# Performance work log

Hardware: AMD Instinct MI355X
Metric: run time of the kernel (lower is better)

## Reference

```python
import jax, jax.numpy as jnp
import numpy as np

P, OBS, H, MSG, EMB, A = 2048, 512, 2048, 16, 32, 3
SLOPE = 0.01  # LeakyReLU default negative slope


def setup_inputs() -> dict:
    key = jax.random.key(0)
    ks = jax.random.split(key, 12)
    s = 0.02
    return {
        "obs": jax.random.normal(ks[0], (P, OBS), jnp.float32),
        "messages": jnp.zeros((P, MSG), jnp.float32),
        "embeddings": jnp.zeros((P, EMB), jnp.float32),
        "h": jnp.zeros((1, H), jnp.float32),
        "w_ih": jax.random.normal(ks[1], (3 * H, OBS), jnp.float32) * s,
        "w_hh": jax.random.normal(ks[2], (3 * H, H), jnp.float32) * s,
        "b_ih": jax.random.normal(ks[3], (3 * H,), jnp.float32) * s,
        "b_hh": jax.random.normal(ks[4], (3 * H,), jnp.float32) * s,
        "ff_w": jax.random.normal(ks[5], (2, H), jnp.float32) * s,
        "ff_b": jnp.zeros((2,), jnp.float32),
        "ap_w": jax.random.normal(ks[6], (A, H), jnp.float32) * s,
        "ap_b": jnp.zeros((A,), jnp.float32),
        "dp_w": jax.random.normal(ks[7], (A, H), jnp.float32) * s,
        "dp_b": jnp.zeros((A,), jnp.float32),
        "v_w": jax.random.normal(ks[8], (1, H), jnp.float32) * s,
        "v_b": jnp.zeros((1,), jnp.float32),
    }


def reference(obs, messages, embeddings, h, w_ih, w_hh, b_ih, b_hh,
              ff_w, ff_b, ap_w, ap_b, dp_w, dp_b, v_w, v_b):
    # h arg is ignored (module re-initializes it to zeros).
    hid = w_hh.shape[1]
    # precompute input-side GRU gates for all players: [P, 3H]
    gi_all = obs @ w_ih.T + b_ih

    def step(hc, gi):  # hc: [H]
        gh = hc @ w_hh.T + b_hh
        ir, iz, inn = jnp.split(gi, 3)
        hr, hz, hn = jnp.split(gh, 3)
        r = jax.nn.sigmoid(ir + hr)
        z = jax.nn.sigmoid(iz + hz)
        n = jnp.tanh(inn + r * hn)
        h_new = (1.0 - z) * n + z * hc
        return h_new, h_new

    h0 = jnp.zeros((hid,), obs.dtype)
    _, hs = jax.lax.scan(step, h0, gi_all)  # [P, H]

    acts = hs @ ff_w.T + ff_b                      # [P, 2]
    acts = jnp.where(acts >= 0, acts, SLOPE * acts)  # LeakyReLU
    a_w = jax.nn.softmax(acts[:, 0])               # softmax over players
    d_w = jax.nn.softmax(acts[:, 1])
    a_att = a_w @ hs                               # [H]
    d_att = d_w @ hs
    a_pol = a_att @ ap_w.T + ap_b
    d_pol = d_att @ dp_w.T + dp_b
    v = (a_att + d_att) @ v_w.T + v_b
    return (a_pol, d_pol, v)
```

## Files before the change

kernel.cpp:

```cpp
#include <hip/hip_runtime.h>
#include <cstdint>
#include <cstddef>

#define P_N  2048
#define OBS_N 512
#define H_N  2048
#define G3H  6144

__device__ __forceinline__ float wave_sum(float v) {
#pragma unroll
  for (int off = 32; off > 0; off >>= 1) v += __shfl_xor(v, off);
  return v;
}
__device__ __forceinline__ float wave_max(float v) {
#pragma unroll
  for (int off = 32; off > 0; off >>= 1) v = fmaxf(v, __shfl_xor(v, off));
  return v;
}

__global__ __launch_bounds__(256, 2) void gi_gemm(
    const float* __restrict__ A,
    const float* __restrict__ B,
    const float* __restrict__ bias,
    float* __restrict__ C)
{
  constexpr int BM = 128, BK = 32, LDP = BM + 4;
  __shared__ float As[BK][LDP];
  __shared__ float Bs[BK][LDP];
  const int tid = threadIdx.x;
  const int bm = blockIdx.y * BM;
  const int bn = blockIdx.x * BM;
  const int tx = tid & 15, ty = tid >> 4;
  const int lrow = tid >> 3;
  const int lk4  = (tid & 7) << 2;

  float acc[8][8];
#pragma unroll
  for (int i = 0; i < 8; ++i)
#pragma unroll
    for (int j = 0; j < 8; ++j) acc[i][j] = 0.f;

  for (int k0 = 0; k0 < OBS_N; k0 += BK) {
#pragma unroll
    for (int i = 0; i < 4; ++i) {
      const int r = lrow + 32 * i;
      float4 av = *(const float4*)(A + (size_t)(bm + r) * OBS_N + k0 + lk4);
      float4 bv = *(const float4*)(B + (size_t)(bn + r) * OBS_N + k0 + lk4);
      As[lk4 + 0][r] = av.x; As[lk4 + 1][r] = av.y;
      As[lk4 + 2][r] = av.z; As[lk4 + 3][r] = av.w;
      Bs[lk4 + 0][r] = bv.x; Bs[lk4 + 1][r] = bv.y;
      Bs[lk4 + 2][r] = bv.z; Bs[lk4 + 3][r] = bv.w;
    }
    __syncthreads();
#pragma unroll
    for (int k = 0; k < BK; ++k) {
      float4 a0 = *(const float4*)&As[k][ty * 4];
      float4 a1 = *(const float4*)&As[k][64 + ty * 4];
      float4 b0 = *(const float4*)&Bs[k][tx * 4];
      float4 b1 = *(const float4*)&Bs[k][64 + tx * 4];
      float a[8] = {a0.x, a0.y, a0.z, a0.w, a1.x, a1.y, a1.z, a1.w};
      float b[8] = {b0.x, b0.y, b0.z, b0.w, b1.x, b1.y, b1.z, b1.w};
#pragma unroll
      for (int i = 0; i < 8; ++i)
#pragma unroll
        for (int j = 0; j < 8; ++j)
          acc[i][j] = fmaf(a[i], b[j], acc[i][j]);
    }
    __syncthreads();
  }

  float4 bs0 = *(const float4*)(bias + bn + tx * 4);
  float4 bs1 = *(const float4*)(bias + bn + 64 + tx * 4);
  const float bb[8] = {bs0.x, bs0.y, bs0.z, bs0.w, bs1.x, bs1.y, bs1.z, bs1.w};
#pragma unroll
  for (int i = 0; i < 8; ++i) {
    const int row = bm + ((i < 4) ? (ty * 4 + i) : (64 + ty * 4 + i - 4));
    float4 o0 = {acc[i][0] + bb[0], acc[i][1] + bb[1], acc[i][2] + bb[2], acc[i][3] + bb[3]};
    float4 o1 = {acc[i][4] + bb[4], acc[i][5] + bb[5], acc[i][6] + bb[6], acc[i][7] + bb[7]};
    *(float4*)(C + (size_t)row * G3H + bn + tx * 4) = o0;
    *(float4*)(C + (size_t)row * G3H + bn + 64 + tx * 4) = o1;
  }
}

#define AGW(reg, val) \
  asm volatile("v_accvgpr_write_b32 " reg ", %0" :: "v"(val) : reg)
#define AGR(reg, dst) \
  asm volatile("v_accvgpr_read_b32 %0, " reg : "=v"(dst) :: reg)

#define LOADK_(koff, r0a,r0b,r0c,r0d, r1a,r1b,r1c,r1d, r2a,r2b,r2c,r2d) do { \
    float4 A_ = *(const float4*)(p0 + (koff) * 256 + l4); \
    float4 B_ = *(const float4*)(p1 + (koff) * 256 + l4); \
    float4 C_ = *(const float4*)(p2 + (koff) * 256 + l4); \
    AGW(r0a, A_.x); AGW(r0b, A_.y); AGW(r0c, A_.z); AGW(r0d, A_.w); \
    AGW(r1a, B_.x); AGW(r1b, B_.y); AGW(r1c, B_.z); AGW(r1d, B_.w); \
    AGW(r2a, C_.x); AGW(r2b, C_.y); AGW(r2c, C_.z); AGW(r2d, C_.w); \
  } while (0)

#define GEMVK_(koff, r0a,r0b,r0c,r0d, r1a,r1b,r1c,r1d, r2a,r2b,r2c,r2d) do { \
    float4 hv = *(const float4*)&hbuf[(koff) * 256 + l4]; \
    float tw; \
    AGR(r0a, tw); acc0 = fmaf(tw, hv.x, acc0); \
    AGR(r0b, tw); acc0 = fmaf(tw, hv.y, acc0); \
    AGR(r0c, tw); acc0 = fmaf(tw, hv.z, acc0); \
    AGR(r0d, tw); acc0 = fmaf(tw, hv.w, acc0); \
    AGR(r1a, tw); acc1 = fmaf(tw, hv.x, acc1); \
    AGR(r1b, tw); acc1 = fmaf(tw, hv.y, acc1); \
    AGR(r1c, tw); acc1 = fmaf(tw, hv.z, acc1); \
    AGR(r1d, tw); acc1 = fmaf(tw, hv.w, acc1); \
    AGR(r2a, tw); acc2 = fmaf(tw, hv.x, acc2); \
    AGR(r2b, tw); acc2 = fmaf(tw, hv.y, acc2); \
    AGR(r2c, tw); acc2 = fmaf(tw, hv.z, acc2); \
    AGR(r2d, tw); acc2 = fmaf(tw, hv.w, acc2); \
  } while (0)

#define LOADK(...) LOADK_(__VA_ARGS__)
#define GEMVK(...) GEMVK_(__VA_ARGS__)

#define KL0 "a0","a1","a2","a3",    "a32","a33","a34","a35", "a64","a65","a66","a67"
#define KL1 "a4","a5","a6","a7",    "a36","a37","a38","a39", "a68","a69","a70","a71"
#define KL2 "a8","a9","a10","a11",  "a40","a41","a42","a43", "a72","a73","a74","a75"
#define KL3 "a12","a13","a14","a15","a44","a45","a46","a47", "a76","a77","a78","a79"
#define KL4 "a16","a17","a18","a19","a48","a49","a50","a51", "a80","a81","a82","a83"
#define KL5 "a20","a21","a22","a23","a52","a53","a54","a55", "a84","a85","a86","a87"
#define KL6 "a24","a25","a26","a27","a56","a57","a58","a59", "a88","a89","a90","a91"
#define KL7 "a28","a29","a30","a31","a60","a61","a62","a63", "a92","a93","a94","a95"

__global__ __launch_bounds__(512, 1) void gru_scan(
    const float* __restrict__ w_hh,
    const float* __restrict__ b_hh,
    const float* __restrict__ gi,
    float* __restrict__ hs,
    unsigned long long* mb)
{
  __shared__ __align__(16) float hbuf[H_N];
  const int g   = blockIdx.x;
  const int tid = threadIdx.x;
  const int w   = tid >> 6;
  const int l   = tid & 63;
  const int l4  = l * 4;
  const int j   = (g << 3) + w;
  const int seg = (w << 8) + l;

  {
    const float* p0 = w_hh + (size_t)j * H_N;
    const float* p1 = w_hh + (size_t)(H_N + j) * H_N;
    const float* p2 = w_hh + (size_t)(2 * H_N + j) * H_N;
    LOADK(0, KL0); LOADK(1, KL1); LOADK(2, KL2); LOADK(3, KL3);
    LOADK(4, KL4); LOADK(5, KL5); LOADK(6, KL6); LOADK(7, KL7);
  }
  const float bh0 = b_hh[j], bh1 = b_hh[H_N + j], bh2 = b_hh[2 * H_N + j];
  float hprev = 0.f;

  for (int t = 0; t < P_N; ++t) {
    const float ir  = gi[(size_t)t * G3H + j];
    const float iz  = gi[(size_t)t * G3H + H_N + j];
    const float inn = gi[(size_t)t * G3H + 2 * H_N + j];

    float acc0 = 0.f, acc1 = 0.f, acc2 = 0.f;
    if (t > 0) {
      const unsigned tag = (unsigned)t;
      unsigned long long* base = mb + (size_t)((t - 1) & 1) * H_N + seg;
      float v0, v1, v2, v3;
      for (;;) {
        unsigned long long a0 =
            __hip_atomic_load(base +   0, __ATOMIC_RELAXED, __HIP_MEMORY_SCOPE_AGENT);
        unsigned long long a1 =
            __hip_atomic_load(base +  64, __ATOMIC_RELAXED, __HIP_MEMORY_SCOPE_AGENT);
        unsigned long long a2 =
            __hip_atomic_load(base + 128, __ATOMIC_RELAXED, __HIP_MEMORY_SCOPE_AGENT);
        unsigned long long a3 =
            __hip_atomic_load(base + 192, __ATOMIC_RELAXED, __HIP_MEMORY_SCOPE_AGENT);
        bool ok = ((unsigned)(a0 >> 32) == tag) & ((unsigned)(a1 >> 32) == tag) &
                  ((unsigned)(a2 >> 32) == tag) & ((unsigned)(a3 >> 32) == tag);
        if (__all(ok)) {
          v0 = __uint_as_float((unsigned)a0);
          v1 = __uint_as_float((unsigned)a1);
          v2 = __uint_as_float((unsigned)a2);
          v3 = __uint_as_float((unsigned)a3);
          break;
        }
        __builtin_amdgcn_s_sleep(1);
      }
      __syncthreads();
      hbuf[seg +   0] = v0;
      hbuf[seg +  64] = v1;
      hbuf[seg + 128] = v2;
      hbuf[seg + 192] = v3;
      __syncthreads();

      if (g == ((t - 1) & 255)) {
        *(float4*)(hs + (size_t)(t - 1) * H_N + tid * 4) =
            *(const float4*)&hbuf[tid * 4];
      }

      GEMVK(0, KL0); GEMVK(1, KL1); GEMVK(2, KL2); GEMVK(3, KL3);
      GEMVK(4, KL4); GEMVK(5, KL5); GEMVK(6, KL6); GEMVK(7, KL7);

#pragma unroll
      for (int off = 32; off > 0; off >>= 1) {
        acc0 += __shfl_xor(acc0, off);
        acc1 += __shfl_xor(acc1, off);
        acc2 += __shfl_xor(acc2, off);
      }
    }

    const float r = 1.f / (1.f + __expf(-(ir + acc0 + bh0)));
    const float z = 1.f / (1.f + __expf(-(iz + acc1 + bh1)));
    const float narg = inn + r * (acc2 + bh2);
    const float e2 = __expf(2.f * narg);
    const float n = (e2 - 1.f) / (e2 + 1.f);
    const float hnew = (1.f - z) * n + z * hprev;
    hprev = hnew;

    if (l == 0) {
      unsigned long long pk = ((unsigned long long)(unsigned)(t + 1) << 32) |
                              (unsigned long long)__float_as_uint(hnew);
      __hip_atomic_store(mb + (size_t)(t & 1) * H_N + j, pk,
                         __ATOMIC_RELAXED, __HIP_MEMORY_SCOPE_AGENT);
    }
  }

  if (l == 0) hs[(size_t)(P_N - 1) * H_N + j] = hprev;
}

__global__ __launch_bounds__(512) void acts_kernel(
    const float* __restrict__ hs, const float* __restrict__ ff_w,
    const float* __restrict__ ff_b, float* __restrict__ acts)
{
  const int w = threadIdx.x >> 6, l = threadIdx.x & 63;
  const int p = blockIdx.x * 8 + w;
  const float* hrow = hs + (size_t)p * H_N;
  float sa = 0.f, sd = 0.f;
#pragma unroll
  for (int k = 0; k < 8; ++k) {
    float4 hv = *(const float4*)(hrow + k * 256 + l * 4);
    float4 fa = *(const float4*)(ff_w + k * 256 + l * 4);
    float4 fd = *(const float4*)(ff_w + H_N + k * 256 + l * 4);
    sa += hv.x * fa.x + hv.y * fa.y + hv.z * fa.z + hv.w * fa.w;
    sd += hv.x * fd.x + hv.y * fd.y + hv.z * fd.z + hv.w * fd.w;
  }
  sa = wave_sum(sa); sd = wave_sum(sd);
  if (l == 0) {
    float a = sa + ff_b[0];
    float d = sd + ff_b[1];
    a = (a >= 0.f) ? a : 0.01f * a;
    d = (d >= 0.f) ? d : 0.01f * d;
    acts[p] = a;
    acts[P_N + p] = d;
  }
}

__global__ __launch_bounds__(256) void softmax_kernel(
    const float* __restrict__ acts, float* __restrict__ wts)
{
  __shared__ float red[4];
  __shared__ float bcast;
  const int tid = threadIdx.x;
  const int w = tid >> 6, l = tid & 63;
  for (int c = 0; c < 2; ++c) {
    const float* x = acts + c * P_N;
    float* y = wts + c * P_N;
    float m = -3.4e38f;
    for (int i = tid; i < P_N; i += 256) m = fmaxf(m, x[i]);
    m = wave_max(m);
    if (l == 0) red[w] = m;
    __syncthreads();
    if (tid == 0) bcast = fmaxf(fmaxf(red[0], red[1]), fmaxf(red[2], red[3]));
    __syncthreads();
    const float M = bcast;
    float s = 0.f;
    for (int i = tid; i < P_N; i += 256) {
      float e = __expf(x[i] - M);
      y[i] = e;
      s += e;
    }
    s = wave_sum(s);
    __syncthreads();
    if (l == 0) red[w] = s;
    __syncthreads();
    if (tid == 0) bcast = 1.f / (red[0] + red[1] + red[2] + red[3]);
    __syncthreads();
    const float inv = bcast;
    for (int i = tid; i < P_N; i += 256) y[i] *= inv;
    __syncthreads();
  }
}

__global__ __launch_bounds__(256) void pool_kernel(
    const float* __restrict__ hs, const float* __restrict__ wts,
    float* __restrict__ att)
{
  const int g = blockIdx.x;
  const int tid = threadIdx.x;
  const int c0 = tid * 8;
  float aa[8] = {0, 0, 0, 0, 0, 0, 0, 0};
  float dd[8] = {0, 0, 0, 0, 0, 0, 0, 0};
  for (int r = 0; r < 16; ++r) {
    const int p = g * 16 + r;
    const float wa = wts[p];
    const float wd = wts[P_N + p];
    const float* hp = hs + (size_t)p * H_N + c0;
    float4 h0 = *(const float4*)hp;
    float4 h1 = *(const float4*)(hp + 4);
    aa[0] = fmaf(wa, h0.x, aa[0]); aa[1] = fmaf(wa, h0.y, aa[1]);
    aa[2] = fmaf(wa, h0.z, aa[2]); aa[3] = fmaf(wa, h0.w, aa[3]);
    aa[4] = fmaf(wa, h1.x, aa[4]); aa[5] = fmaf(wa, h1.y, aa[5]);
    aa[6] = fmaf(wa, h1.z, aa[6]); aa[7] = fmaf(wa, h1.w, aa[7]);
    dd[0] = fmaf(wd, h0.x, dd[0]); dd[1] = fmaf(wd, h0.y, dd[1]);
    dd[2] = fmaf(wd, h0.z, dd[2]); dd[3] = fmaf(wd, h0.w, dd[3]);
    dd[4] = fmaf(wd, h1.x, dd[4]); dd[5] = fmaf(wd, h1.y, dd[5]);
    dd[6] = fmaf(wd, h1.z, dd[6]); dd[7] = fmaf(wd, h1.w, dd[7]);
  }
#pragma unroll
  for (int q = 0; q < 8; ++q) {
    atomicAdd(&att[c0 + q], aa[q]);
    atomicAdd(&att[H_N + c0 + q], dd[q]);
  }
}

__global__ __launch_bounds__(512) void head_kernel(
    const float* __restrict__ att,
    const float* __restrict__ ap_w, const float* __restrict__ ap_b,
    const float* __restrict__ dp_w, const float* __restrict__ dp_b,
    const float* __restrict__ v_w, const float* __restrict__ v_b,
    float* __restrict__ out)
{
  const int w = threadIdx.x >> 6, l = threadIdx.x & 63;
  if (w >= 7) return;
  float s = 0.f;
  if (w < 3) {
    const float* m = ap_w + (size_t)w * H_N;
    for (int k = 0; k < 32; ++k) { int i = k * 64 + l; s += att[i] * m[i]; }
  } else if (w < 6) {
    const float* m = dp_w + (size_t)(w - 3) * H_N;
    for (int k = 0; k < 32; ++k) { int i = k * 64 + l; s += att[H_N + i] * m[i]; }
  } else {
    for (int k = 0; k < 32; ++k) { int i = k * 64 + l; s += (att[i] + att[H_N + i]) * v_w[i]; }
  }
  s = wave_sum(s);
  if (l == 0) {
    float b = (w < 3) ? ap_b[w] : ((w < 6) ? dp_b[w - 3] : v_b[0]);
    out[w] = s + b;
  }
}

extern "C" void kernel_launch(void* const* d_in, const int* in_sizes, int n_in,
                              void* d_out, int out_size, void* d_ws, size_t ws_size,
                              hipStream_t stream) {
  const float* obs  = (const float*)d_in[0];
  const float* w_ih = (const float*)d_in[4];
  const float* w_hh = (const float*)d_in[5];
  const float* b_ih = (const float*)d_in[6];
  const float* b_hh = (const float*)d_in[7];
  const float* ff_w = (const float*)d_in[8];
  const float* ff_b = (const float*)d_in[9];
  const float* ap_w = (const float*)d_in[10];
  const float* ap_b = (const float*)d_in[11];
  const float* dp_w = (const float*)d_in[12];
  const float* dp_b = (const float*)d_in[13];
  const float* v_w  = (const float*)d_in[14];
  const float* v_b  = (const float*)d_in[15];
  float* out = (float*)d_out;

  float* gi = (float*)d_ws;
  float* hs = gi + (size_t)P_N * G3H;
  unsigned long long* mb = (unsigned long long*)(hs + (size_t)P_N * H_N);
  float* acts = (float*)(mb + 2 * H_N);
  float* wts  = acts + 2 * P_N;
  float* att  = wts + 2 * P_N;

  hipMemsetAsync(mb, 0, 2 * H_N * sizeof(unsigned long long), stream);
  hipMemsetAsync(att, 0, 2 * H_N * sizeof(float), stream);

  gi_gemm<<<dim3(G3H / 128, P_N / 128), 256, 0, stream>>>(obs, w_ih, b_ih, gi);
  gru_scan<<<256, 512, 0, stream>>>(w_hh, b_hh, gi, hs, mb);
  acts_kernel<<<P_N / 8, 512, 0, stream>>>(hs, ff_w, ff_b, acts);
  softmax_kernel<<<1, 256, 0, stream>>>(acts, wts);
  pool_kernel<<<128, 256, 0, stream>>>(hs, wts, att);
  head_kernel<<<1, 512, 0, stream>>>(att, ap_w, ap_b, dp_w, dp_b, v_w, v_b, out);
}
```

Before: 9.788 ms.

## Add per-block ready flags and double-buffer hidden state in GRU scan

Each block now publishes a per-block flag once all 8 of its waves have stored their hidden values. Only wave 0 polls the 256 flags with system-coherent loads, then signals the other waves through a shared-memory variable. The hidden-state LDS buffer is double-buffered by step parity, which removes one __syncthreads per step. The goal is to cut polling traffic on the mailbox and barrier overhead on the serial critical path, at the cost of an extra flag hop and a shared atomic counter.

```diff
diff --git a/kernel.cpp b/kernel.cpp
--- a/kernel.cpp
+++ b/kernel.cpp
@@ -6,6 +6,8 @@
 #define OBS_N 512
 #define H_N  2048
 #define G3H  6144
+
+typedef unsigned uint4v __attribute__((ext_vector_type(4)));
 
 __device__ __forceinline__ float wave_sum(float v) {
 #pragma unroll
@@ -97,7 +99,7 @@
   } while (0)
 
 #define GEMVK_(koff, r0a,r0b,r0c,r0d, r1a,r1b,r1c,r1d, r2a,r2b,r2c,r2d) do { \
-    float4 hv = *(const float4*)&hbuf[(koff) * 256 + l4]; \
+    float4 hv = *(const float4*)&hb[(koff) * 256 + l4]; \
     float tw; \
     AGR(r0a, tw); acc0 = fmaf(tw, hv.x, acc0); \
     AGR(r0b, tw); acc0 = fmaf(tw, hv.y, acc0); \
@@ -130,9 +132,12 @@
     const float* __restrict__ b_hh,
     const float* __restrict__ gi,
     float* __restrict__ hs,
-    unsigned long long* mb)
-{
-  __shared__ __align__(16) float hbuf[H_N];
+    unsigned long long* mb,
+    unsigned* flags)
+{
+  __shared__ __align__(16) float hbuf[2][H_N];
+  __shared__ volatile int ready;
+  __shared__ unsigned pubcnt;
   const int g   = blockIdx.x;
   const int tid = threadIdx.x;
   const int w   = tid >> 6;
@@ -141,6 +146,8 @@
   const int j   = (g << 3) + w;
   const int seg = (w << 8) + l;
 
+  if (tid == 0) { ready = 0; pubcnt = 0u; }
+
   {
     const float* p0 = w_hh + (size_t)j * H_N;
     const float* p1 = w_hh + (size_t)(H_N + j) * H_N;
@@ -150,6 +157,7 @@
   }
   const float bh0 = b_hh[j], bh1 = b_hh[H_N + j], bh2 = b_hh[2 * H_N + j];
   float hprev = 0.f;
+  __syncthreads();
 
   for (int t = 0; t < P_N; ++t) {
     const float ir  = gi[(size_t)t * G3H + j];
@@ -159,7 +167,25 @@
     float acc0 = 0.f, acc1 = 0.f, acc2 = 0.f;
     if (t > 0) {
       const unsigned tag = (unsigned)t;
-      unsigned long long* base = mb + (size_t)((t - 1) & 1) * H_N + seg;
+      const int par = (t - 1) & 1;
+
+      if (w == 0) {
+        const unsigned* fp = flags + (size_t)par * 256 + (l << 2);
+        for (;;) {
+          uint4v f;
+          asm volatile("global_load_dwordx4 %0, %1, off sc0 sc1\n\t"
+                       "s_waitcnt vmcnt(0)"
+                       : "=v"(f) : "v"(fp) : "memory");
+          bool ok = (f.x >= tag) & (f.y >= tag) & (f.z >= tag) & (f.w >= tag);
+          if (__all(ok)) break;
+          __builtin_amdgcn_s_sleep(1);
+        }
+        if (l == 0) ready = t;
+      } else {
+        while (ready < t) __builtin_amdgcn_s_sleep(1);
+      }
+
+      unsigned long long* base = mb + (size_t)par * H_N + seg;
       float v0, v1, v2, v3;
       for (;;) {
         unsigned long long a0 =
@@ -181,18 +207,18 @@
         }
         __builtin_amdgcn_s_sleep(1);
       }
-      __syncthreads();
-      hbuf[seg +   0] = v0;
-      hbuf[seg +  64] = v1;
-      hbuf[seg + 128] = v2;
-      hbuf[seg + 192] = v3;
+      hbuf[par][seg +   0] = v0;
+      hbuf[par][seg +  64] = v1;
+      hbuf[par][seg + 128] = v2;
+      hbuf[par][seg + 192] = v3;
       __syncthreads();
 
       if (g == ((t - 1) & 255)) {
         *(float4*)(hs + (size_t)(t - 1) * H_N + tid * 4) =
-            *(const float4*)&hbuf[tid * 4];
+            *(const float4*)&hbuf[par][tid * 4];
       }
 
+      const float* hb = &hbuf[par][0];
       GEMVK(0, KL0); GEMVK(1, KL1); GEMVK(2, KL2); GEMVK(3, KL3);
       GEMVK(4, KL4); GEMVK(5, KL5); GEMVK(6, KL6); GEMVK(7, KL7);
 
@@ -217,6 +243,11 @@
                               (unsigned long long)__float_as_uint(hnew);
       __hip_atomic_store(mb + (size_t)(t & 1) * H_N + j, pk,
                          __ATOMIC_RELAXED, __HIP_MEMORY_SCOPE_AGENT);
+      unsigned old = atomicAdd(&pubcnt, 1u);
+      if (old == 8u * (unsigned)t + 7u) {
+        __hip_atomic_store(flags + (size_t)(t & 1) * 256 + g, (unsigned)(t + 1),
+                           __ATOMIC_RELAXED, __HIP_MEMORY_SCOPE_AGENT);
+      }
     }
   }
 
@@ -365,15 +396,16 @@
   float* gi = (float*)d_ws;
   float* hs = gi + (size_t)P_N * G3H;
   unsigned long long* mb = (unsigned long long*)(hs + (size_t)P_N * H_N);
-  float* acts = (float*)(mb + 2 * H_N);
+  unsigned* flags = (unsigned*)(mb + 2 * H_N);
+  float* acts = (float*)(flags + 2 * 256);
   float* wts  = acts + 2 * P_N;
   float* att  = wts + 2 * P_N;
 
-  hipMemsetAsync(mb, 0, 2 * H_N * sizeof(unsigned long long), stream);
+  hipMemsetAsync(mb, 0, 2 * H_N * sizeof(unsigned long long) + 2 * 256 * sizeof(unsigned), stream);
   hipMemsetAsync(att, 0, 2 * H_N * sizeof(float), stream);
 
   gi_gemm<<<dim3(G3H / 128, P_N / 128), 256, 0, stream>>>(obs, w_ih, b_ih, gi);
-  gru_scan<<<256, 512, 0, stream>>>(w_hh, b_hh, gi, hs, mb);
+  gru_scan<<<256, 512, 0, stream>>>(w_hh, b_hh, gi, hs, mb, flags);
   acts_kernel<<<P_N / 8, 512, 0, stream>>>(hs, ff_w, ff_b, acts);
   softmax_kernel<<<1, 256, 0, stream>>>(acts, wts);
   pool_kernel<<<128, 256, 0, stream>>>(hs, wts, att);
```

Result: no change. 9.891 ms (+1.1%).
